# Kernel optimization log

Measured on AMD Instinct MI355X. Metric: run time of the kernel, lower is better.

Reference implementation:

```python
import jax, jax.numpy as jnp
import numpy as np

A, B = 8192, 8192
E1, E2, C = 1024, 1024, 1024
M = min(E1, E2)


def setup_inputs() -> dict:
    key = jax.random.key(0)
    ks = jax.random.split(key, 9)
    s = lambda fan_in: 1.0 / np.sqrt(fan_in)
    return {
        "seq1_ae": jax.random.normal(ks[0], (A, E1), jnp.float32),
        "seq2_be": jax.random.normal(ks[1], (B, E2), jnp.float32),
        "context_c": jax.random.normal(ks[2], (C,), jnp.float32),
        "W_ctx1": jax.random.uniform(ks[3], (M, C), jnp.float32, -s(C), s(C)),
        "W_ctx2": jax.random.uniform(ks[4], (M, C), jnp.float32, -s(C), s(C)),
        "W1": jax.random.uniform(ks[5], (M, E1), jnp.float32, -s(E1), s(E1)),
        "b1": jax.random.uniform(ks[6], (M,), jnp.float32, -s(E1), s(E1)),
        "W2": jax.random.uniform(ks[7], (M, E2), jnp.float32, -s(E2), s(E2)),
        "b2": jax.random.uniform(ks[8], (M,), jnp.float32, -s(E2), s(E2)),
    }


def reference(seq1_ae, seq2_be, context_c, W_ctx1, W_ctx2, W1, b1, W2, b2):
    ctx1_m = W_ctx1 @ context_c                      # [m]
    ctx2_m = W_ctx2 @ context_c                      # [m]
    p1_am = jax.nn.elu(seq1_ae @ W1.T + b1 + ctx1_m) # [a, m]
    p2_bm = jax.nn.elu(seq2_be @ W2.T + b2 + ctx2_m) # [b, m]
    matrix_ab = p1_am @ p2_bm.T                      # [a, b]
    logits_a = matrix_ab.sum(1)                      # [a]
    logits_b = matrix_ab.sum(0)                      # [b]
    att1 = seq1_ae.T @ jax.nn.softmax(logits_a)      # [e1]
    att2 = seq2_be.T @ jax.nn.softmax(logits_b)      # [e2]
    return (att1, att2)
```

## Files before the change

### kernel.cpp

```cpp
#include <hip/hip_runtime.h>
#include <hip/hip_bf16.h>


#define A_ROWS 8192
#define EDIM   1024
#define MDIM   1024

typedef __attribute__((ext_vector_type(8))) short bf16x8;
typedef __attribute__((ext_vector_type(4))) int i32x4;

#define OFF_BIAS1   0ull
#define OFF_BIAS2   4096ull
#define OFF_S1      8192ull
#define OFF_S2      12288ull
#define OFF_LOGA    16384ull
#define OFF_P1      81920ull
#define OFF_P2      (OFF_P1 + 16777216ull)
#define OFF_SEQ1B   (OFF_P2 + 16777216ull)
#define OFF_SEQ2B   (OFF_SEQ1B + 16777216ull)
#define OFF_W1B     (OFF_SEQ2B + 16777216ull)
#define OFF_W2B     (OFF_W1B + 2097152ull)

#define SA_INV 21.166666f
#define SW_INV 4064.0f
#define SP_INV 25.4f
#define DQ_P   (5.0f / 127.0f)
#define DQ_A   (6.0f / 127.0f)

__device__ __forceinline__ unsigned pack4(float4 f, float s) {
  int q0 = __float2int_rn(f.x * s); q0 = q0 > 127 ? 127 : (q0 < -127 ? -127 : q0);
  int q1 = __float2int_rn(f.y * s); q1 = q1 > 127 ? 127 : (q1 < -127 ? -127 : q1);
  int q2 = __float2int_rn(f.z * s); q2 = q2 > 127 ? 127 : (q2 < -127 ? -127 : q2);
  int q3 = __float2int_rn(f.w * s); q3 = q3 > 127 ? 127 : (q3 < -127 ? -127 : q3);
  return (q0 & 255) | ((q1 & 255) << 8) | ((q2 & 255) << 16) | ((q3 & 255) << 24);
}

#define GLOAD16(src, dst) __builtin_amdgcn_global_load_lds( \
    (const __attribute__((address_space(1))) void*)(src),   \
    (__attribute__((address_space(3))) void*)(dst), 16, 0, 0)

__global__ __launch_bounds__(256) void prep_k(
    const float* __restrict__ s1, const float* __restrict__ s2,
    const float* __restrict__ w1, const float* __restrict__ w2,
    uint2* __restrict__ s1o, uint2* __restrict__ s2o,
    uint2* __restrict__ w1o, uint2* __restrict__ w2o,
    const float* __restrict__ Wc1, const float* __restrict__ Wc2,
    const float* __restrict__ ctx, const float* __restrict__ b1,
    const float* __restrict__ b2, float* __restrict__ bias1,
    float* __restrict__ bias2, float* __restrict__ S1, float* __restrict__ S2,
    float* __restrict__ outz) {
  int z = blockIdx.z;
  if (z < 4) {
    const float* in = z == 0 ? s1 : z == 1 ? s2 : z == 2 ? w1 : w2;
    uint2* out = z == 0 ? s1o : z == 1 ? s2o : z == 2 ? w1o : w2o;
    float sc = z < 2 ? SA_INV : SW_INV;
    int n8 = z < 2 ? (A_ROWS * EDIM / 8) : (MDIM * EDIM / 8);
    int stride = gridDim.x * blockDim.x;
    for (int i = blockIdx.x * blockDim.x + threadIdx.x; i < n8; i += stride) {
      float4 fa = reinterpret_cast<const float4*>(in)[2 * i];
      float4 fb = reinterpret_cast<const float4*>(in)[2 * i + 1];
      out[i] = make_uint2(pack4(fa, sc), pack4(fb, sc));
    }
  } else {
    if (blockIdx.x == 0) {
      float4 zv = make_float4(0.f, 0.f, 0.f, 0.f);
      ((float4*)outz)[threadIdx.x] = zv;
      ((float4*)outz)[threadIdx.x + 256] = zv;
    }
    if (blockIdx.x >= 512) return;
    int zz = blockIdx.x >= 256;
    int bx = blockIdx.x & 255;
    const float* W = zz ? Wc2 : Wc1;
    const float* b = zz ? b2 : b1;
    float* bias = zz ? bias2 : bias1;
    float* S = zz ? S2 : S1;
    int wave = threadIdx.x >> 6, lane = threadIdx.x & 63;
    int m = bx * 4 + wave;
    const float4* wr = reinterpret_cast<const float4*>(W + (size_t)m * EDIM);
    const float4* cv = reinterpret_cast<const float4*>(ctx);
    float acc = 0.f;
#pragma unroll
    for (int ch = 0; ch < 4; ++ch) {
      float4 a = wr[ch * 64 + lane], d = cv[ch * 64 + lane];
      acc += a.x * d.x + a.y * d.y + a.z * d.z + a.w * d.w;
    }
    for (int o = 32; o; o >>= 1) acc += __shfl_down(acc, o);
    if (lane == 0) { bias[m] = acc + b[m]; S[m] = 0.f; }
  }
}

__global__ __launch_bounds__(512) void gemm8(
    const char* __restrict__ A1, const char* __restrict__ A2,
    const char* __restrict__ B1, const char* __restrict__ B2,
    const float* __restrict__ bias1, const float* __restrict__ bias2,
    char* __restrict__ P1, char* __restrict__ P2,
    float* __restrict__ S1, float* __restrict__ S2) {
  const int z = blockIdx.z;
  const char* __restrict__ Ab = z ? A2 : A1;
  const char* __restrict__ Bb = z ? B2 : B1;
  const float* __restrict__ bias = z ? bias2 : bias1;
  char* __restrict__ P = z ? P2 : P1;
  float* __restrict__ S = z ? S2 : S1;

  __shared__ ushort lds[65536];
  char* ldsb = (char*)lds;

  const int tid = threadIdx.x;
  const int lane = tid & 63;
  const int wave = tid >> 6;
  const int wm = wave >> 2, wn = wave & 3;
  const int r = lane & 15, kq = lane >> 4;
  const int brow = blockIdx.x * 256, bcol = blockIdx.y * 256;

  const int swzr = ((r >> 1) & 3) << 4;
  const int aRd = wm * 8192 + r * 64 + ((kq * 16) ^ swzr);
  const int bRd = 32768 + wn * 4096 + r * 64 + ((kq * 16) ^ swzr);

  const int srow = tid >> 2;
  const int sswz = ((srow >> 1) & 3) << 4;
  const char* aSrc = Ab + (size_t)(brow + srow) * 1024 + (((tid & 3) * 16) ^ sswz);
  const char* bSrc = Bb + (size_t)(bcol + srow) * 1024 + (((tid & 3) * 16) ^ sswz);

#define STG_A(buf, half, kt) GLOAD16(aSrc + (half) * 131072 + (kt) * 64, \
    ldsb + (buf) * 16384 + (half) * 8192 + tid * 16)
#define STG_B(buf, half, kt) GLOAD16(bSrc + (half) * 131072 + (kt) * 64, \
    ldsb + 32768 + (buf) * 16384 + (half) * 8192 + tid * 16)
#define RDA(buf, mf) (*(const i32x4*)(ldsb + aRd + (buf) * 16384 + (mf) * 1024))
#define RDB(buf, nf) (*(const i32x4*)(ldsb + bRd + (buf) * 16384 + (nf) * 1024))
#define VMW2 asm volatile("s_waitcnt vmcnt(2)" ::: "memory")
#define VMW0 asm volatile("s_waitcnt vmcnt(0)" ::: "memory")
#define BAR __builtin_amdgcn_s_barrier()
#define MF(a, b, c) __builtin_amdgcn_mfma_i32_16x16x64_i8((a), (b), (c), 0, 0, 0)
#define LDB4(buf) do { b0 = RDB(buf, 0); b1 = RDB(buf, 1); \
    b2 = RDB(buf, 2); b3 = RDB(buf, 3); } while (0)
#define LDA4(buf, m0) do { a0 = RDA(buf, (m0)); a1 = RDA(buf, (m0) + 1); \
    a2 = RDA(buf, (m0) + 2); a3 = RDA(buf, (m0) + 3); } while (0)
#define MM(q) do { __builtin_amdgcn_s_setprio(1); \
    acc[(q)+0][0] = MF(a0, b0, acc[(q)+0][0]); acc[(q)+0][1] = MF(a0, b1, acc[(q)+0][1]); \
    acc[(q)+0][2] = MF(a0, b2, acc[(q)+0][2]); acc[(q)+0][3] = MF(a0, b3, acc[(q)+0][3]); \
    acc[(q)+1][0] = MF(a1, b0, acc[(q)+1][0]); acc[(q)+1][1] = MF(a1, b1, acc[(q)+1][1]); \
    acc[(q)+1][2] = MF(a1, b2, acc[(q)+1][2]); acc[(q)+1][3] = MF(a1, b3, acc[(q)+1][3]); \
    acc[(q)+2][0] = MF(a2, b0, acc[(q)+2][0]); acc[(q)+2][1] = MF(a2, b1, acc[(q)+2][1]); \
    acc[(q)+2][2] = MF(a2, b2, acc[(q)+2][2]); acc[(q)+2][3] = MF(a2, b3, acc[(q)+2][3]); \
    acc[(q)+3][0] = MF(a3, b0, acc[(q)+3][0]); acc[(q)+3][1] = MF(a3, b1, acc[(q)+3][1]); \
    acc[(q)+3][2] = MF(a3, b2, acc[(q)+3][2]); acc[(q)+3][3] = MF(a3, b3, acc[(q)+3][3]); \
    __builtin_amdgcn_s_setprio(0); } while (0)

  i32x4 acc[8][4] = {};
  i32x4 a0, a1, a2, a3, b0, b1, b2, b3;

  STG_A(0, 0, 0); STG_A(0, 1, 0); STG_B(0, 0, 0); STG_B(0, 1, 0);
  STG_B(1, 0, 1); STG_B(1, 1, 1);

  for (int it = 0; it < 7; ++it) {
    const int k1 = 2 * it + 1, k2 = 2 * it + 2, k3 = 2 * it + 3;
    VMW2; BAR;
    LDB4(0); LDA4(0, 0); STG_A(1, 0, k1); STG_A(1, 1, k1); MM(0);
    BAR;
    LDA4(0, 4); STG_B(0, 0, k2); STG_B(0, 1, k2); MM(4);
    VMW2; BAR;
    LDB4(1); LDA4(1, 0); STG_A(0, 0, k2); STG_A(0, 1, k2); MM(0);
    BAR;
    LDA4(1, 4); STG_B(1, 0, k3); STG_B(1, 1, k3); MM(4);
  }
  VMW2; BAR;
  LDB4(0); LDA4(0, 0); STG_A(1, 0, 15); STG_A(1, 1, 15); MM(0);
  BAR;
  LDA4(0, 4); MM(4);
  VMW0; BAR;
  LDB4(1); LDA4(1, 0); MM(0);
  BAR;
  LDA4(1, 4); MM(4);
  BAR;

  const float DQ = (6.0f / 127.0f) * (0.03125f / 127.0f);
  const int wcol = wn * 64, wrow = wm * 128;
  char* pl = (char*)lds;
  float bv[4], cs[4] = {0.f, 0.f, 0.f, 0.f};
#pragma unroll
  for (int nf = 0; nf < 4; ++nf) bv[nf] = bias[bcol + wcol + nf * 16 + r];
#pragma unroll
  for (int mf = 0; mf < 8; ++mf)
#pragma unroll
    for (int nf = 0; nf < 4; ++nf)
#pragma unroll
      for (int j = 0; j < 4; ++j) {
        float v = (float)acc[mf][nf][j] * DQ + bv[nf];
        v = v > 0.f ? v : (__expf(v) - 1.f);
        cs[nf] += v;
        int q = __float2int_rn(v * SP_INV);
        q = q > 127 ? 127 : (q < -127 ? -127 : q);
        int row = wrow + mf * 16 + kq * 4 + j;
        pl[row * 256 + wcol + nf * 16 + r] = (char)q;
      }
#pragma unroll
  for (int nf = 0; nf < 4; ++nf) {
    cs[nf] += __shfl_xor(cs[nf], 16);
    cs[nf] += __shfl_xor(cs[nf], 32);
    if (kq == 0) atomicAdd(&S[bcol + wcol + nf * 16 + r], cs[nf]);
  }
  __syncthreads();
#pragma unroll
  for (int i = 0; i < 8; ++i) {
    int c = i * 512 + tid;
    int row = c >> 4, coff = (c & 15) * 16;
    *(uint4*)(P + (size_t)(brow + row) * MDIM + bcol + coff) =
        *(const uint4*)(pl + row * 256 + coff);
  }
#undef STG_A
#undef STG_B
#undef RDA
#undef RDB
#undef VMW2
#undef VMW0
#undef BAR
#undef MF
#undef LDB4
#undef LDA4
#undef MM
}

__global__ __launch_bounds__(256) void gemv_logits_k(
    const char* __restrict__ P1, const char* __restrict__ P2,
    const float* __restrict__ S1, const float* __restrict__ S2,
    float* __restrict__ L) {
  int z = blockIdx.z;
  const char* P = z ? P2 : P1;
  const float* s = z ? S1 : S2;
  float* Lz = L + (size_t)z * 8192;
  int wave = threadIdx.x >> 6, lane = threadIdx.x & 63;
  int row = blockIdx.x * 4 + wave;
  uint4 w = *(const uint4*)(P + (size_t)row * MDIM + lane * 16);
  const float4* sv = reinterpret_cast<const float4*>(s + lane * 16);
  float4 s0 = sv[0], s1v = sv[1], s2v = sv[2], s3v = sv[3];
  float acc =
      (float)(char)(w.x) * s0.x + (float)(char)(w.x >> 8) * s0.y +
      (float)(char)(w.x >> 16) * s0.z + (float)(char)(w.x >> 24) * s0.w +
      (float)(char)(w.y) * s1v.x + (float)(char)(w.y >> 8) * s1v.y +
      (float)(char)(w.y >> 16) * s1v.z + (float)(char)(w.y >> 24) * s1v.w +
      (float)(char)(w.z) * s2v.x + (float)(char)(w.z >> 8) * s2v.y +
      (float)(char)(w.z >> 16) * s2v.z + (float)(char)(w.z >> 24) * s2v.w +
      (float)(char)(w.w) * s3v.x + (float)(char)(w.w >> 8) * s3v.y +
      (float)(char)(w.w >> 16) * s3v.z + (float)(char)(w.w >> 24) * s3v.w;
  for (int o = 32; o; o >>= 1) acc += __shfl_down(acc, o);
  if (lane == 0) Lz[row] = acc * DQ_P;
}

__global__ __launch_bounds__(256) void att_sm_k(const char* __restrict__ s1b,
    const char* __restrict__ s2b, const float* __restrict__ logits,
    float* __restrict__ out) {
  int z = blockIdx.z;
  const char* seq = z ? s2b : s1b;
  const float* L = logits + (size_t)z * 8192;
  float* o = out + (size_t)z * EDIM;
  __shared__ float red[256];
  __shared__ float wsm[128];
  int tid = threadIdx.x;

  float lv[32];
  float m = -3.4e38f;
#pragma unroll
  for (int k = 0; k < 32; ++k) { lv[k] = L[tid + k * 256]; m = fmaxf(m, lv[k]); }
  red[tid] = m; __syncthreads();
  for (int s = 128; s; s >>= 1) {
    if (tid < s) red[tid] = fmaxf(red[tid], red[tid + s]);
    __syncthreads();
  }
  m = red[0]; __syncthreads();
  float sum = 0.f;
#pragma unroll
  for (int k = 0; k < 32; ++k) sum += __expf(lv[k] - m);
  red[tid] = sum; __syncthreads();
  for (int s = 128; s; s >>= 1) {
    if (tid < s) red[tid] += red[tid + s];
    __syncthreads();
  }
  float inv = 1.f / red[0];

  int a0 = blockIdx.y * 128;
  if (tid < 128) wsm[tid] = __expf(L[a0 + tid] - m) * inv;
  __syncthreads();

  float c0 = 0.f, c1 = 0.f, c2 = 0.f, c3 = 0.f;
  const char* p = seq + (size_t)a0 * EDIM + tid * 4;
#pragma unroll 4
  for (int j = 0; j < 128; ++j, p += EDIM) {
    float wa = wsm[j];
    unsigned v = *reinterpret_cast<const unsigned*>(p);
    c0 += wa * (float)(char)(v);
    c1 += wa * (float)(char)(v >> 8);
    c2 += wa * (float)(char)(v >> 16);
    c3 += wa * (float)(char)(v >> 24);
  }
  atomicAdd(&o[tid * 4 + 0], c0 * DQ_A);
  atomicAdd(&o[tid * 4 + 1], c1 * DQ_A);
  atomicAdd(&o[tid * 4 + 2], c2 * DQ_A);
  atomicAdd(&o[tid * 4 + 3], c3 * DQ_A);
}

extern "C" void kernel_launch(void* const* d_in, const int* in_sizes, int n_in,
                              void* d_out, int out_size, void* d_ws, size_t ws_size,
                              hipStream_t stream) {
  const float* seq1 = (const float*)d_in[0];
  const float* seq2 = (const float*)d_in[1];
  const float* ctx  = (const float*)d_in[2];
  const float* Wc1  = (const float*)d_in[3];
  const float* Wc2  = (const float*)d_in[4];
  const float* W1   = (const float*)d_in[5];
  const float* b1   = (const float*)d_in[6];
  const float* W2   = (const float*)d_in[7];
  const float* b2   = (const float*)d_in[8];
  float* out = (float*)d_out;
  char* ws = (char*)d_ws;

  float* bias1 = (float*)(ws + OFF_BIAS1);
  float* bias2 = (float*)(ws + OFF_BIAS2);
  float* s1    = (float*)(ws + OFF_S1);
  float* s2    = (float*)(ws + OFF_S2);
  float* loga  = (float*)(ws + OFF_LOGA);
  char* p1     = (char*)(ws + OFF_P1);
  char* p2     = (char*)(ws + OFF_P2);
  char* seq1b  = (char*)(ws + OFF_SEQ1B);
  char* seq2b  = (char*)(ws + OFF_SEQ2B);
  char* w1b    = (char*)(ws + OFF_W1B);
  char* w2b    = (char*)(ws + OFF_W2B);

  prep_k<<<dim3(512, 1, 5), 256, 0, stream>>>(
      seq1, seq2, W1, W2, (uint2*)seq1b, (uint2*)seq2b, (uint2*)w1b, (uint2*)w2b,
      Wc1, Wc2, ctx, b1, b2, bias1, bias2, s1, s2, out);

  gemm8<<<dim3(A_ROWS / 256, MDIM / 256, 2), 512, 0, stream>>>(
      seq1b, seq2b, w1b, w2b, bias1, bias2, p1, p2, s1, s2);

  gemv_logits_k<<<dim3(2048, 1, 2), 256, 0, stream>>>(p1, p2, s1, s2, loga);

  att_sm_k<<<dim3(1, 64, 2), 256, 0, stream>>>(seq1b, seq2b, loga, out);
}
```

Baseline: 68.25 us.

## Double the int8 GEMM K-tile to 128 and restage the LDS pipeline

The int8 projection GEMM now stages 128-byte K tiles instead of 64, using the full 128KB LDS for double-buffered A and B tiles. The swizzle is widened to 8 rows, and each stage issues two 16-byte global-to-LDS loads per thread. The main loop now has 8 K iterations split into four barrier phases, each doing two chained MFMAs per accumulator. The aim is to halve the number of pipeline stages and barriers per unit of MFMA work. The cost is more registers for B fragments, more barriers inside each stage, and a larger LDS footprint.

```diff
diff --git a/kernel.cpp b/kernel.cpp
--- a/kernel.cpp
+++ b/kernel.cpp
@@ -112,65 +112,72 @@
   const int r = lane & 15, kq = lane >> 4;
   const int brow = blockIdx.x * 256, bcol = blockIdx.y * 256;
 
-  const int swzr = ((r >> 1) & 3) << 4;
-  const int aRd = wm * 8192 + r * 64 + ((kq * 16) ^ swzr);
-  const int bRd = 32768 + wn * 4096 + r * 64 + ((kq * 16) ^ swzr);
-
-  const int srow = tid >> 2;
-  const int sswz = ((srow >> 1) & 3) << 4;
-  const char* aSrc = Ab + (size_t)(brow + srow) * 1024 + (((tid & 3) * 16) ^ sswz);
-  const char* bSrc = Bb + (size_t)(bcol + srow) * 1024 + (((tid & 3) * 16) ^ sswz);
-
-#define STG_A(buf, half, kt) GLOAD16(aSrc + (half) * 131072 + (kt) * 64, \
-    ldsb + (buf) * 16384 + (half) * 8192 + tid * 16)
-#define STG_B(buf, half, kt) GLOAD16(bSrc + (half) * 131072 + (kt) * 64, \
-    ldsb + 32768 + (buf) * 16384 + (half) * 8192 + tid * 16)
-#define RDA(buf, mf) (*(const i32x4*)(ldsb + aRd + (buf) * 16384 + (mf) * 1024))
-#define RDB(buf, nf) (*(const i32x4*)(ldsb + bRd + (buf) * 16384 + (nf) * 1024))
-#define VMW2 asm volatile("s_waitcnt vmcnt(2)" ::: "memory")
+  const int swz = (r & 7) << 4;
+  const int aRd0 = (wm * 128 + r) * 128 + ((kq * 16) ^ swz);
+  const int aRd1 = (wm * 128 + r) * 128 + ((64 + kq * 16) ^ swz);
+  const int bRd0 = 65536 + (wn * 64 + r) * 128 + ((kq * 16) ^ swz);
+  const int bRd1 = 65536 + (wn * 64 + r) * 128 + ((64 + kq * 16) ^ swz);
+
+  const int srow = tid >> 3;
+  const int sbyte = ((tid & 7) * 16) ^ ((srow & 7) << 4);
+  const char* aSrc = Ab + (size_t)(brow + srow) * 1024 + sbyte;
+  const char* bSrc = Bb + (size_t)(bcol + srow) * 1024 + sbyte;
+
+#define STG_A(buf, h, kt) do { \
+    const char* s_ = aSrc + (h) * 131072 + (kt) * 128; \
+    char* d_ = ldsb + (buf) * 32768 + (h) * 16384 + tid * 16; \
+    GLOAD16(s_, d_); GLOAD16(s_ + 65536, d_ + 8192); } while (0)
+#define STG_B(buf, h, kt) do { \
+    const char* s_ = bSrc + (h) * 131072 + (kt) * 128; \
+    char* d_ = ldsb + 65536 + (buf) * 32768 + (h) * 16384 + tid * 16; \
+    GLOAD16(s_, d_); GLOAD16(s_ + 65536, d_ + 8192); } while (0)
+#define RDA(buf, mf, s) (*(const i32x4*)(ldsb + ((s) ? aRd1 : aRd0) + (buf) * 32768 + (mf) * 2048))
+#define RDB(buf, nf, s) (*(const i32x4*)(ldsb + ((s) ? bRd1 : bRd0) + (buf) * 32768 + (nf) * 2048))
+#define VMW4 asm volatile("s_waitcnt vmcnt(4)" ::: "memory")
 #define VMW0 asm volatile("s_waitcnt vmcnt(0)" ::: "memory")
 #define BAR __builtin_amdgcn_s_barrier()
 #define MF(a, b, c) __builtin_amdgcn_mfma_i32_16x16x64_i8((a), (b), (c), 0, 0, 0)
-#define LDB4(buf) do { b0 = RDB(buf, 0); b1 = RDB(buf, 1); \
-    b2 = RDB(buf, 2); b3 = RDB(buf, 3); } while (0)
-#define LDA4(buf, m0) do { a0 = RDA(buf, (m0)); a1 = RDA(buf, (m0) + 1); \
-    a2 = RDA(buf, (m0) + 2); a3 = RDA(buf, (m0) + 3); } while (0)
-#define MM(q) do { __builtin_amdgcn_s_setprio(1); \
-    acc[(q)+0][0] = MF(a0, b0, acc[(q)+0][0]); acc[(q)+0][1] = MF(a0, b1, acc[(q)+0][1]); \
-    acc[(q)+0][2] = MF(a0, b2, acc[(q)+0][2]); acc[(q)+0][3] = MF(a0, b3, acc[(q)+0][3]); \
-    acc[(q)+1][0] = MF(a1, b0, acc[(q)+1][0]); acc[(q)+1][1] = MF(a1, b1, acc[(q)+1][1]); \
-    acc[(q)+1][2] = MF(a1, b2, acc[(q)+1][2]); acc[(q)+1][3] = MF(a1, b3, acc[(q)+1][3]); \
-    acc[(q)+2][0] = MF(a2, b0, acc[(q)+2][0]); acc[(q)+2][1] = MF(a2, b1, acc[(q)+2][1]); \
-    acc[(q)+2][2] = MF(a2, b2, acc[(q)+2][2]); acc[(q)+2][3] = MF(a2, b3, acc[(q)+2][3]); \
-    acc[(q)+3][0] = MF(a3, b0, acc[(q)+3][0]); acc[(q)+3][1] = MF(a3, b1, acc[(q)+3][1]); \
-    acc[(q)+3][2] = MF(a3, b2, acc[(q)+3][2]); acc[(q)+3][3] = MF(a3, b3, acc[(q)+3][3]); \
+#define LDB_ALL(buf) do { \
+    b00 = RDB(buf, 0, 0); b01 = RDB(buf, 0, 1); b10 = RDB(buf, 1, 0); b11 = RDB(buf, 1, 1); \
+    b20 = RDB(buf, 2, 0); b21 = RDB(buf, 2, 1); b30 = RDB(buf, 3, 0); b31 = RDB(buf, 3, 1); } while (0)
+#define LDA2(buf, m0) do { a00 = RDA(buf, (m0), 0); a01 = RDA(buf, (m0), 1); \
+    a10 = RDA(buf, (m0) + 1, 0); a11 = RDA(buf, (m0) + 1, 1); } while (0)
+#define MM2(q) do { __builtin_amdgcn_s_setprio(1); \
+    acc[q][0] = MF(a00, b00, acc[q][0]); acc[q][0] = MF(a01, b01, acc[q][0]); \
+    acc[q][1] = MF(a00, b10, acc[q][1]); acc[q][1] = MF(a01, b11, acc[q][1]); \
+    acc[q][2] = MF(a00, b20, acc[q][2]); acc[q][2] = MF(a01, b21, acc[q][2]); \
+    acc[q][3] = MF(a00, b30, acc[q][3]); acc[q][3] = MF(a01, b31, acc[q][3]); \
+    acc[(q)+1][0] = MF(a10, b00, acc[(q)+1][0]); acc[(q)+1][0] = MF(a11, b01, acc[(q)+1][0]); \
+    acc[(q)+1][1] = MF(a10, b10, acc[(q)+1][1]); acc[(q)+1][1] = MF(a11, b11, acc[(q)+1][1]); \
+    acc[(q)+1][2] = MF(a10, b20, acc[(q)+1][2]); acc[(q)+1][2] = MF(a11, b21, acc[(q)+1][2]); \
+    acc[(q)+1][3] = MF(a10, b30, acc[(q)+1][3]); acc[(q)+1][3] = MF(a11, b31, acc[(q)+1][3]); \
     __builtin_amdgcn_s_setprio(0); } while (0)
 
   i32x4 acc[8][4] = {};
-  i32x4 a0, a1, a2, a3, b0, b1, b2, b3;
-
-  STG_A(0, 0, 0); STG_A(0, 1, 0); STG_B(0, 0, 0); STG_B(0, 1, 0);
+  i32x4 a00, a01, a10, a11;
+  i32x4 b00, b01, b10, b11, b20, b21, b30, b31;
+
+  STG_B(0, 0, 0); STG_B(0, 1, 0); STG_A(0, 0, 0); STG_A(0, 1, 0);
   STG_B(1, 0, 1); STG_B(1, 1, 1);
 
-  for (int it = 0; it < 7; ++it) {
-    const int k1 = 2 * it + 1, k2 = 2 * it + 2, k3 = 2 * it + 3;
-    VMW2; BAR;
-    LDB4(0); LDA4(0, 0); STG_A(1, 0, k1); STG_A(1, 1, k1); MM(0);
-    BAR;
-    LDA4(0, 4); STG_B(0, 0, k2); STG_B(0, 1, k2); MM(4);
-    VMW2; BAR;
-    LDB4(1); LDA4(1, 0); STG_A(0, 0, k2); STG_A(0, 1, k2); MM(0);
-    BAR;
-    LDA4(1, 4); STG_B(1, 0, k3); STG_B(1, 1, k3); MM(4);
-  }
-  VMW2; BAR;
-  LDB4(0); LDA4(0, 0); STG_A(1, 0, 15); STG_A(1, 1, 15); MM(0);
-  BAR;
-  LDA4(0, 4); MM(4);
+  for (int kt = 0; kt < 6; ++kt) {
+    const int buf = kt & 1;
+    VMW4; BAR;
+    LDB_ALL(buf); LDA2(buf, 0); STG_A(buf ^ 1, 0, kt + 1); MM2(0);
+    BAR; LDA2(buf, 2); STG_A(buf ^ 1, 1, kt + 1); MM2(2);
+    BAR; LDA2(buf, 4); STG_B(buf, 0, kt + 2); MM2(4);
+    BAR; LDA2(buf, 6); STG_B(buf, 1, kt + 2); MM2(6);
+  }
+  VMW4; BAR;
+  LDB_ALL(0); LDA2(0, 0); STG_A(1, 0, 7); MM2(0);
+  BAR; LDA2(0, 2); STG_A(1, 1, 7); MM2(2);
+  BAR; LDA2(0, 4); MM2(4);
+  BAR; LDA2(0, 6); MM2(6);
   VMW0; BAR;
-  LDB4(1); LDA4(1, 0); MM(0);
-  BAR;
-  LDA4(1, 4); MM(4);
+  LDB_ALL(1); LDA2(1, 0); MM2(0);
+  BAR; LDA2(1, 2); MM2(2);
+  BAR; LDA2(1, 4); MM2(4);
+  BAR; LDA2(1, 6); MM2(6);
   BAR;
 
   const float DQ = (6.0f / 127.0f) * (0.03125f / 127.0f);
@@ -211,13 +218,13 @@
 #undef STG_B
 #undef RDA
 #undef RDB
-#undef VMW2
+#undef VMW4
 #undef VMW0
 #undef BAR
 #undef MF
-#undef LDB4
-#undef LDA4
-#undef MM
+#undef LDB_ALL
+#undef LDA2
+#undef MM2
 }
 
 __global__ __launch_bounds__(256) void gemv_logits_k(
```

New measurement: 67.70 us. About the same (-0.8%).

## Shrink int8 GEMM tile to 256x128 and reduce column sums in LDS

Applied to the files above, without the earlier changes.

The ELU-projection int8 GEMM tile shrinks from 256x256 to 256x128. Each wave now computes a 64x64 sub-tile with half the accumulators, and a launch-bounds hint asks for higher occupancy. The K loop becomes a simpler two-stage double buffer with LDS reduced to about 48KB. Column sums are first combined across waves in LDS, so only one global atomic per column per block is issued. The aim is more resident waves and twice the grid size, for better latency hiding and fuller CU use, at the cost of less operand reuse per block.

```diff
diff --git a/kernel.cpp b/kernel.cpp
--- a/kernel.cpp
+++ b/kernel.cpp
@@ -89,7 +89,7 @@
   }
 }
 
-__global__ __launch_bounds__(512) void gemm8(
+__global__ __launch_bounds__(512, 4) void gemm8(
     const char* __restrict__ A1, const char* __restrict__ A2,
     const char* __restrict__ B1, const char* __restrict__ B2,
     const float* __restrict__ bias1, const float* __restrict__ bias2,
@@ -102,85 +102,80 @@
   char* __restrict__ P = z ? P2 : P1;
   float* __restrict__ S = z ? S2 : S1;
 
-  __shared__ ushort lds[65536];
-  char* ldsb = (char*)lds;
+  __shared__ __align__(16) char ldsb[49664];
+  float* scol = (float*)(ldsb + 49152);
 
   const int tid = threadIdx.x;
   const int lane = tid & 63;
   const int wave = tid >> 6;
-  const int wm = wave >> 2, wn = wave & 3;
+  const int wm = wave >> 1, wn = wave & 1;
   const int r = lane & 15, kq = lane >> 4;
-  const int brow = blockIdx.x * 256, bcol = blockIdx.y * 256;
-
-  const int swzr = ((r >> 1) & 3) << 4;
-  const int aRd = wm * 8192 + r * 64 + ((kq * 16) ^ swzr);
-  const int bRd = 32768 + wn * 4096 + r * 64 + ((kq * 16) ^ swzr);
+  const int brow = blockIdx.x * 256, bcol = blockIdx.y * 128;
+
+  const int swz = ((r >> 1) & 3) << 4;
+  const int kb = (kq * 16) ^ swz;
+  const int aRd = (wm * 64 + r) * 64 + kb;
+  const int bRd = 32768 + (wn * 64 + r) * 64 + kb;
 
   const int srow = tid >> 2;
-  const int sswz = ((srow >> 1) & 3) << 4;
-  const char* aSrc = Ab + (size_t)(brow + srow) * 1024 + (((tid & 3) * 16) ^ sswz);
-  const char* bSrc = Bb + (size_t)(bcol + srow) * 1024 + (((tid & 3) * 16) ^ sswz);
-
-#define STG_A(buf, half, kt) GLOAD16(aSrc + (half) * 131072 + (kt) * 64, \
-    ldsb + (buf) * 16384 + (half) * 8192 + tid * 16)
-#define STG_B(buf, half, kt) GLOAD16(bSrc + (half) * 131072 + (kt) * 64, \
-    ldsb + 32768 + (buf) * 16384 + (half) * 8192 + tid * 16)
+  const int sbyte = ((tid & 3) * 16) ^ (((srow >> 1) & 3) << 4);
+  const char* aSrc = Ab + (size_t)(brow + srow) * 1024 + sbyte;
+  const char* bSrc = Bb + (size_t)(bcol + srow) * 1024 + sbyte;
+
+#define STG_A(buf, kt) do { \
+    const char* s_ = aSrc + (kt) * 64; \
+    char* d_ = ldsb + (buf) * 16384 + tid * 16; \
+    GLOAD16(s_, d_); GLOAD16(s_ + 131072, d_ + 8192); } while (0)
+#define STG_B(buf, kt) GLOAD16(bSrc + (kt) * 64, ldsb + 32768 + (buf) * 8192 + tid * 16)
 #define RDA(buf, mf) (*(const i32x4*)(ldsb + aRd + (buf) * 16384 + (mf) * 1024))
-#define RDB(buf, nf) (*(const i32x4*)(ldsb + bRd + (buf) * 16384 + (nf) * 1024))
-#define VMW2 asm volatile("s_waitcnt vmcnt(2)" ::: "memory")
+#define RDB(buf, nf) (*(const i32x4*)(ldsb + bRd + (buf) * 8192 + (nf) * 1024))
+#define VMW3 asm volatile("s_waitcnt vmcnt(3)" ::: "memory")
 #define VMW0 asm volatile("s_waitcnt vmcnt(0)" ::: "memory")
 #define BAR __builtin_amdgcn_s_barrier()
 #define MF(a, b, c) __builtin_amdgcn_mfma_i32_16x16x64_i8((a), (b), (c), 0, 0, 0)
-#define LDB4(buf) do { b0 = RDB(buf, 0); b1 = RDB(buf, 1); \
+#define LDB_ALL(buf) do { b0 = RDB(buf, 0); b1 = RDB(buf, 1); \
     b2 = RDB(buf, 2); b3 = RDB(buf, 3); } while (0)
-#define LDA4(buf, m0) do { a0 = RDA(buf, (m0)); a1 = RDA(buf, (m0) + 1); \
-    a2 = RDA(buf, (m0) + 2); a3 = RDA(buf, (m0) + 3); } while (0)
-#define MM(q) do { __builtin_amdgcn_s_setprio(1); \
-    acc[(q)+0][0] = MF(a0, b0, acc[(q)+0][0]); acc[(q)+0][1] = MF(a0, b1, acc[(q)+0][1]); \
-    acc[(q)+0][2] = MF(a0, b2, acc[(q)+0][2]); acc[(q)+0][3] = MF(a0, b3, acc[(q)+0][3]); \
-    acc[(q)+1][0] = MF(a1, b0, acc[(q)+1][0]); acc[(q)+1][1] = MF(a1, b1, acc[(q)+1][1]); \
-    acc[(q)+1][2] = MF(a1, b2, acc[(q)+1][2]); acc[(q)+1][3] = MF(a1, b3, acc[(q)+1][3]); \
-    acc[(q)+2][0] = MF(a2, b0, acc[(q)+2][0]); acc[(q)+2][1] = MF(a2, b1, acc[(q)+2][1]); \
-    acc[(q)+2][2] = MF(a2, b2, acc[(q)+2][2]); acc[(q)+2][3] = MF(a2, b3, acc[(q)+2][3]); \
-    acc[(q)+3][0] = MF(a3, b0, acc[(q)+3][0]); acc[(q)+3][1] = MF(a3, b1, acc[(q)+3][1]); \
-    acc[(q)+3][2] = MF(a3, b2, acc[(q)+3][2]); acc[(q)+3][3] = MF(a3, b3, acc[(q)+3][3]); \
-    __builtin_amdgcn_s_setprio(0); } while (0)
-
-  i32x4 acc[8][4] = {};
-  i32x4 a0, a1, a2, a3, b0, b1, b2, b3;
-
-  STG_A(0, 0, 0); STG_A(0, 1, 0); STG_B(0, 0, 0); STG_B(0, 1, 0);
-  STG_B(1, 0, 1); STG_B(1, 1, 1);
-
-  for (int it = 0; it < 7; ++it) {
-    const int k1 = 2 * it + 1, k2 = 2 * it + 2, k3 = 2 * it + 3;
-    VMW2; BAR;
-    LDB4(0); LDA4(0, 0); STG_A(1, 0, k1); STG_A(1, 1, k1); MM(0);
+#define MMQ(q, a_) do { \
+    acc[q][0] = MF(a_, b0, acc[q][0]); acc[q][1] = MF(a_, b1, acc[q][1]); \
+    acc[q][2] = MF(a_, b2, acc[q][2]); acc[q][3] = MF(a_, b3, acc[q][3]); } while (0)
+
+  i32x4 acc[4][4] = {};
+  i32x4 a0, a1, b0, b1, b2, b3;
+
+  STG_A(0, 0); STG_B(0, 0); STG_A(1, 1); STG_B(1, 1);
+
+  for (int kt = 0; kt < 14; ++kt) {
+    const int buf = kt & 1;
+    VMW3; BAR;
+    LDB_ALL(buf); a0 = RDA(buf, 0); a1 = RDA(buf, 1);
+    __builtin_amdgcn_s_setprio(1); MMQ(0, a0); MMQ(1, a1); __builtin_amdgcn_s_setprio(0);
     BAR;
-    LDA4(0, 4); STG_B(0, 0, k2); STG_B(0, 1, k2); MM(4);
-    VMW2; BAR;
-    LDB4(1); LDA4(1, 0); STG_A(0, 0, k2); STG_A(0, 1, k2); MM(0);
+    a0 = RDA(buf, 2); a1 = RDA(buf, 3);
+    __builtin_amdgcn_s_setprio(1); MMQ(2, a0); MMQ(3, a1); __builtin_amdgcn_s_setprio(0);
     BAR;
-    LDA4(1, 4); STG_B(1, 0, k3); STG_B(1, 1, k3); MM(4);
-  }
-  VMW2; BAR;
-  LDB4(0); LDA4(0, 0); STG_A(1, 0, 15); STG_A(1, 1, 15); MM(0);
+    STG_A(buf, kt + 2); STG_B(buf, kt + 2);
+  }
+  VMW3; BAR;
+  LDB_ALL(0); a0 = RDA(0, 0); a1 = RDA(0, 1);
+  __builtin_amdgcn_s_setprio(1); MMQ(0, a0); MMQ(1, a1); __builtin_amdgcn_s_setprio(0);
   BAR;
-  LDA4(0, 4); MM(4);
+  a0 = RDA(0, 2); a1 = RDA(0, 3);
+  __builtin_amdgcn_s_setprio(1); MMQ(2, a0); MMQ(3, a1); __builtin_amdgcn_s_setprio(0);
   VMW0; BAR;
-  LDB4(1); LDA4(1, 0); MM(0);
+  LDB_ALL(1); a0 = RDA(1, 0); a1 = RDA(1, 1);
+  __builtin_amdgcn_s_setprio(1); MMQ(0, a0); MMQ(1, a1); __builtin_amdgcn_s_setprio(0);
   BAR;
-  LDA4(1, 4); MM(4);
+  a0 = RDA(1, 2); a1 = RDA(1, 3);
+  __builtin_amdgcn_s_setprio(1); MMQ(2, a0); MMQ(3, a1); __builtin_amdgcn_s_setprio(0);
   BAR;
 
   const float DQ = (6.0f / 127.0f) * (0.03125f / 127.0f);
-  const int wcol = wn * 64, wrow = wm * 128;
-  char* pl = (char*)lds;
+  const int cl = wn * 64 + r;
   float bv[4], cs[4] = {0.f, 0.f, 0.f, 0.f};
 #pragma unroll
-  for (int nf = 0; nf < 4; ++nf) bv[nf] = bias[bcol + wcol + nf * 16 + r];
-#pragma unroll
-  for (int mf = 0; mf < 8; ++mf)
+  for (int nf = 0; nf < 4; ++nf) bv[nf] = bias[bcol + wn * 64 + nf * 16 + r];
+#pragma unroll
+  for (int mf = 0; mf < 4; ++mf)
 #pragma unroll
     for (int nf = 0; nf < 4; ++nf)
 #pragma unroll
@@ -190,34 +185,46 @@
         cs[nf] += v;
         int q = __float2int_rn(v * SP_INV);
         q = q > 127 ? 127 : (q < -127 ? -127 : q);
-        int row = wrow + mf * 16 + kq * 4 + j;
-        pl[row * 256 + wcol + nf * 16 + r] = (char)q;
+        int row = wm * 64 + mf * 16 + kq * 4 + j;
+        ldsb[row * 128 + wn * 64 + nf * 16 + r] = (char)q;
       }
 #pragma unroll
   for (int nf = 0; nf < 4; ++nf) {
     cs[nf] += __shfl_xor(cs[nf], 16);
     cs[nf] += __shfl_xor(cs[nf], 32);
-    if (kq == 0) atomicAdd(&S[bcol + wcol + nf * 16 + r], cs[nf]);
+  }
+  if (wm == 0 && kq == 0) {
+#pragma unroll
+    for (int nf = 0; nf < 4; ++nf) scol[wn * 64 + nf * 16 + r] = cs[nf];
   }
   __syncthreads();
-#pragma unroll
-  for (int i = 0; i < 8; ++i) {
+  if (wm != 0 && kq == 0) {
+#pragma unroll
+    for (int nf = 0; nf < 4; ++nf) atomicAdd(&scol[wn * 64 + nf * 16 + r], cs[nf]);
+  }
+#pragma unroll
+  for (int i = 0; i < 4; ++i) {
     int c = i * 512 + tid;
-    int row = c >> 4, coff = (c & 15) * 16;
+    int row = c >> 3, coff = (c & 7) * 16;
     *(uint4*)(P + (size_t)(brow + row) * MDIM + bcol + coff) =
-        *(const uint4*)(pl + row * 256 + coff);
+        *(const uint4*)(ldsb + row * 128 + coff);
+  }
+  __syncthreads();
+  if (wm == 0 && kq == 0) {
+#pragma unroll
+    for (int nf = 0; nf < 4; ++nf)
+      atomicAdd(&S[bcol + wn * 64 + nf * 16 + r], scol[wn * 64 + nf * 16 + r]);
   }
 #undef STG_A
 #undef STG_B
 #undef RDA
 #undef RDB
-#undef VMW2
+#undef VMW3
 #undef VMW0
 #undef BAR
 #undef MF
-#undef LDB4
-#undef LDA4
-#undef MM
+#undef LDB_ALL
+#undef MMQ
 }
 
 __global__ __launch_bounds__(256) void gemv_logits_k(
@@ -329,7 +336,7 @@
       seq1, seq2, W1, W2, (uint2*)seq1b, (uint2*)seq2b, (uint2*)w1b, (uint2*)w2b,
       Wc1, Wc2, ctx, b1, b2, bias1, bias2, s1, s2, out);
 
-  gemm8<<<dim3(A_ROWS / 256, MDIM / 256, 2), 512, 0, stream>>>(
+  gemm8<<<dim3(A_ROWS / 256, MDIM / 128, 2), 512, 0, stream>>>(
       seq1b, seq2b, w1b, w2b, bias1, bias2, p1, p2, s1, s2);
 
   gemv_logits_k<<<dim3(2048, 1, 2), 256, 0, stream>>>(p1, p2, s1, s2, loga);
```

Result: no change. 69.38 us (+1.7%).
